# Kernel optimization log

Measured on AMD Instinct MI355X. Metric: run time of the kernel, lower is better.

The kernel has to match this reference:

```python
import jax, jax.numpy as jnp
import numpy as np

EPS = 1e-5
NPOINT, RADIUS, NSAMPLE, HEADS, DH = 512, 0.2, 64, 8, 64


def _ln(x, g, b):
    m = jnp.mean(x, -1, keepdims=True)
    v = jnp.var(x, -1, keepdims=True)
    return (x - m) * jax.lax.rsqrt(v + EPS) * g + b


def _gather(points, idx):
    # points [B,N,C], idx [B,...] -> [B,...,C]
    b = jnp.arange(points.shape[0]).reshape((-1,) + (1,) * (idx.ndim - 1))
    return points[b, idx]


def _fps(xyz, npoint):
    # farthest point sampling, deterministic start at index 0
    B, N, _ = xyz.shape

    def step(carry, _):
        dist, far = carry
        cen = jnp.take_along_axis(xyz, far[:, None, None], axis=1)  # [B,1,3]
        d = jnp.sum((xyz - cen) ** 2, -1)  # [B,N]
        dist = jnp.minimum(dist, d)
        nxt = jnp.argmax(dist, -1).astype(jnp.int32)
        return (dist, nxt), far

    init = (jnp.full((B, N), 1e10, xyz.dtype), jnp.zeros((B,), jnp.int32))
    _, idxs = jax.lax.scan(step, init, None, length=npoint)
    return idxs.T  # [B,npoint]


def _ball_query(xyz, new_xyz):
    # xyz [B,N,3], new_xyz [B,S,3] -> idx [B,S,NSAMPLE]
    N = xyz.shape[1]
    sq = (jnp.sum(new_xyz ** 2, -1)[:, :, None] + jnp.sum(xyz ** 2, -1)[:, None, :]
          - 2.0 * jnp.einsum('bsc,bnc->bsn', new_xyz, xyz))  # [B,S,N]
    gidx = jnp.broadcast_to(jnp.arange(N), sq.shape)
    gidx = jnp.where(sq > RADIUS ** 2, N, gidx)
    neg, _ = jax.lax.top_k(-gidx, NSAMPLE)  # smallest NSAMPLE valid indices
    idx = -neg
    return jnp.where(idx == N, idx[:, :, :1], idx)


def reference(features, sa_w0, sa_b0, sa_w1, sa_b1, sa_w2, sa_b2,
              bn_g0, bn_b0, bn_m0, bn_v0, bn_g1, bn_b1, bn_m1, bn_v1,
              bn_g2, bn_b2, bn_m2, bn_v2,
              lift_w, lift_b, lift_g, lift_beta, cls_token,
              qkv_w, out_w, out_b, ln1_g, ln1_b,
              pe_w1, pe_b1, pe_w2, pe_b2, ln2_g, ln2_b,
              ff_w1, ff_b1, ff_w2, ff_b2):
    B = features.shape[0]
    dim = cls_token.shape[0]
    xyz = jnp.transpose(features, (0, 2, 1))  # [B,N,3] (in_dim=3 so points==xyz)
    pts = xyz

    # ---- PointNet set abstraction ----
    fps_idx = _fps(xyz, NPOINT)
    new_xyz = _gather(xyz, fps_idx)  # [B,S,3]
    idx = _ball_query(xyz, new_xyz)  # [B,S,K]
    g_xyz = _gather(xyz, idx)  # [B,S,K,3]
    g_norm = g_xyz - new_xyz[:, :, None, :]
    g_pts = _gather(pts, idx)
    h = jnp.concatenate([g_norm, g_pts], -1)  # [B,S,K,6]
    h = jnp.transpose(h, (0, 3, 2, 1))  # [B,C,K,S]
    for (w, bb, g, be, m, v) in ((sa_w0, sa_b0, bn_g0, bn_b0, bn_m0, bn_v0),
                                 (sa_w1, sa_b1, bn_g1, bn_b1, bn_m1, bn_v1),
                                 (sa_w2, sa_b2, bn_g2, bn_b2, bn_m2, bn_v2)):
        h = jnp.einsum('bcks,oc->boks', h, w) + bb[None, :, None, None]
        h = (h - m[None, :, None, None]) * jax.lax.rsqrt(v[None, :, None, None] + EPS) \
            * g[None, :, None, None] + be[None, :, None, None]
        h = jax.nn.relu(h)
    feat = jnp.max(h, axis=2)  # [B,sa_dim,S]
    cent = jnp.transpose(new_xyz, (0, 2, 1))  # [B,3,S]

    # ---- lift ----
    x = jnp.einsum('bcs,oc->bos', jnp.concatenate([cent, feat], 1), lift_w) + lift_b[None, :, None]
    x = jnp.transpose(x, (0, 2, 1))  # [B,S,dim]
    x = _ln(x, lift_g, lift_beta)

    # ---- cls token + centroid deltas ----
    x = jnp.concatenate([jnp.broadcast_to(cls_token, (B, 1, dim)), x], 1)  # [B,n,dim]
    cent = jnp.concatenate([jnp.zeros((B, 3, 1), x.dtype), cent], -1)  # [B,3,n]
    delta = cent[:, :, :, None] - cent[:, :, None, :]  # [B,3,n,n]

    # ---- transformer ----
    scale = DH ** -0.5
    depth = qkv_w.shape[0]
    n = x.shape[1]
    for l in range(depth):
        h1 = _ln(x, ln1_g[l], ln1_b[l])
        qkv = h1 @ qkv_w[l]  # [B,n,3*inner]
        q, k, v = jnp.split(qkv, 3, -1)
        q = q.reshape(B, n, HEADS, DH).transpose(0, 2, 1, 3)
        k = k.reshape(B, n, HEADS, DH).transpose(0, 2, 1, 3)
        v = v.reshape(B, n, HEADS, DH).transpose(0, 2, 1, 3)
        pe = jax.nn.relu(jnp.einsum('bcij,oc->boij', delta, pe_w1[l]) + pe_b1[l][None, :, None, None])
        pe = jnp.einsum('bcij,oc->boij', pe, pe_w2[l]) + pe_b2[l][None, :, None, None]  # [B,1,n,n]
        dots = (jnp.einsum('bhid,bhjd->bhij', q, k) + pe) * scale
        attn = jax.nn.softmax(dots, -1)
        o = jnp.einsum('bhij,bhjd->bhid', attn, v).transpose(0, 2, 1, 3).reshape(B, n, HEADS * DH)
        x = x + (o @ out_w[l] + out_b[l])
        h2 = _ln(x, ln2_g[l], ln2_b[l])
        x = x + (jax.nn.gelu(h2 @ ff_w1[l] + ff_b1[l], approximate=False) @ ff_w2[l] + ff_b2[l])
    return x[:, 0]


def setup_inputs() -> dict:
    key = jax.random.key(0)
    ks = iter(jax.random.split(key, 64))

    def rnd(shape, s=0.02):
        return (jax.random.normal(next(ks), shape, jnp.float32) * s)

    D, dim, inner, mlp, sad = 6, 512, 512, 1024, 256
    inp = {}
    inp['features'] = jax.random.uniform(next(ks), (2, 3, 10000), jnp.float32, -1.0, 1.0)
    inp['sa_w0'] = rnd((64, 6), 0.2); inp['sa_b0'] = jnp.zeros((64,), jnp.float32)
    inp['sa_w1'] = rnd((64, 64), 0.1); inp['sa_b1'] = jnp.zeros((64,), jnp.float32)
    inp['sa_w2'] = rnd((sad, 64), 0.1); inp['sa_b2'] = jnp.zeros((sad,), jnp.float32)
    for i, c in ((0, 64), (1, 64), (2, sad)):
        inp[f'bn_g{i}'] = jnp.ones((c,), jnp.float32)
        inp[f'bn_b{i}'] = jnp.zeros((c,), jnp.float32)
        inp[f'bn_m{i}'] = jnp.zeros((c,), jnp.float32)
        inp[f'bn_v{i}'] = jnp.ones((c,), jnp.float32)
    inp['lift_w'] = rnd((dim, sad + 3), 0.05)
    inp['lift_b'] = jnp.zeros((dim,), jnp.float32)
    inp['lift_g'] = jnp.ones((dim,), jnp.float32)
    inp['lift_beta'] = jnp.zeros((dim,), jnp.float32)
    inp['cls_token'] = rnd((dim,), 1.0)
    inp['qkv_w'] = rnd((D, dim, 3 * inner))
    inp['out_w'] = rnd((D, inner, dim))
    inp['out_b'] = jnp.zeros((D, dim), jnp.float32)
    inp['ln1_g'] = jnp.ones((D, dim), jnp.float32)
    inp['ln1_b'] = jnp.zeros((D, dim), jnp.float32)
    inp['pe_w1'] = rnd((D, 64, 3), 0.1)
    inp['pe_b1'] = jnp.zeros((D, 64), jnp.float32)
    inp['pe_w2'] = rnd((D, 1, 64), 0.1)
    inp['pe_b2'] = jnp.zeros((D, 1), jnp.float32)
    inp['ln2_g'] = jnp.ones((D, dim), jnp.float32)
    inp['ln2_b'] = jnp.zeros((D, dim), jnp.float32)
    inp['ff_w1'] = rnd((D, dim, mlp))
    inp['ff_b1'] = jnp.zeros((D, mlp), jnp.float32)
    inp['ff_w2'] = rnd((D, mlp, dim))
    inp['ff_b2'] = jnp.zeros((D, dim), jnp.float32)
    return inp
```

## Files before the change

kernel.cpp:

```cpp
#include <hip/hip_runtime.h>
#include <math.h>

#define NPTS 10000
#define NP   512
#define NS   64
#define NTOK 513
#define DIM  512
#define NHEADS 8
#define DH   64
#define DEPTH 6
#define SAD  256
#define MLPD 1024
#define EPSV 1e-5f
#define PEB  2057

typedef float  f32x2  __attribute__((ext_vector_type(2)));
typedef float  f32x4  __attribute__((ext_vector_type(4)));
typedef __bf16 bf16x8 __attribute__((ext_vector_type(8)));
typedef unsigned short u16x4 __attribute__((ext_vector_type(4)));
typedef unsigned short u16x8 __attribute__((ext_vector_type(8)));

__device__ __forceinline__ unsigned short f2bf(float x) {
    unsigned u = __float_as_uint(x);
    unsigned r = u + 0x7fffu + ((u >> 16) & 1u);
    return (unsigned short)(r >> 16);
}
__device__ __forceinline__ bf16x8 bf8_from_f32(const float* p) {
    u16x8 h;
    #pragma unroll
    for (int e = 0; e < 8; e++) h[e] = f2bf(p[e]);
    return *(bf16x8*)&h;
}

__device__ __forceinline__ float blk_sum256(float v, float* red) {
    #pragma unroll
    for (int off = 32; off; off >>= 1) v += __shfl_down(v, off);
    __syncthreads();
    if ((threadIdx.x & 63) == 0) red[threadIdx.x >> 6] = v;
    __syncthreads();
    return red[0] + red[1] + red[2] + red[3];
}

__global__ __launch_bounds__(512, 1) void fps_wconv_kernel(
        const float* __restrict__ f, float* __restrict__ cent3,
        const float* __restrict__ qkv_w, unsigned short* __restrict__ qkvT,
        const float* __restrict__ out_w, unsigned short* __restrict__ outT,
        const float* __restrict__ ff_w1, unsigned short* __restrict__ ff1T,
        const float* __restrict__ ff_w2, unsigned short* __restrict__ ff2T) {
    #pragma clang fp contract(off)
    __shared__ union {
        struct {
            float pts[3 * 10240];
            unsigned long long spk[2][8];
        } fps;
        unsigned short tl[64][65];
    } sh;

    if (blockIdx.x >= 2) {
        int id = blockIdx.x - 2;
        const float* Ws; unsigned short* Wd; int K, N, tn, per;
        if (id < 1152)      { Ws = qkv_w; Wd = qkvT; K = 512;  N = 1536; tn = 24; per = 192; }
        else if (id < 1536) { id -= 1152; Ws = out_w; Wd = outT; K = 512; N = 512; tn = 8;  per = 64;  }
        else if (id < 2304) { id -= 1536; Ws = ff_w1; Wd = ff1T; K = 512; N = 1024; tn = 16; per = 128; }
        else                { id -= 2304; Ws = ff_w2; Wd = ff2T; K = 1024; N = 512; tn = 8;  per = 128; }
        const int l = id / per, rem = id % per;
        const int n0 = (rem % tn) * 64, k0 = (rem / tn) * 64;
        Ws += (size_t)l * K * N;
        Wd += (size_t)l * K * N;
        const int ty = threadIdx.x >> 4, c4 = (threadIdx.x & 15) * 4;
        #pragma unroll
        for (int i = 0; i < 2; i++) {
            int r = ty + 32 * i;
            f32x4 v = *(const f32x4*)(Ws + (size_t)(k0 + r) * N + n0 + c4);
            sh.tl[c4 + 0][r] = f2bf(v.x);
            sh.tl[c4 + 1][r] = f2bf(v.y);
            sh.tl[c4 + 2][r] = f2bf(v.z);
            sh.tl[c4 + 3][r] = f2bf(v.w);
        }
        __syncthreads();
        #pragma unroll
        for (int i = 0; i < 2; i++) {
            int r = ty + 32 * i;
            u16x4 hv = { sh.tl[r][c4], sh.tl[r][c4 + 1], sh.tl[r][c4 + 2], sh.tl[r][c4 + 3] };
            *(u16x4*)(Wd + (size_t)(n0 + r) * K + k0 + c4) = hv;
        }
        return;
    }

    const int b = blockIdx.x;
    const float* fx = f + (size_t)b * 3 * NPTS;
    const float* fy = fx + NPTS;
    const float* fz = fx + 2 * NPTS;
    const int t = threadIdx.x;
    const int wv = t >> 6, lane = t & 63;

    float* lx = sh.fps.pts;
    float* ly = sh.fps.pts + 10240;
    float* lz = sh.fps.pts + 20480;
    for (int p = t; p < NPTS; p += 512) {
        lx[p] = fx[p]; ly[p] = fy[p]; lz[p] = fz[p];
    }

    f32x2 px[10], py[10], pz[10], dist[10];
    #pragma unroll
    for (int q = 0; q < 10; q++) {
        #pragma unroll
        for (int e = 0; e < 2; e++) {
            int p = t + (2 * q + e) * 512;
            if (p < NPTS) { px[q][e] = fx[p]; py[q][e] = fy[p]; pz[q][e] = fz[p]; dist[q][e] = 1e10f; }
            else          { px[q][e] = 0.f;  py[q][e] = 0.f;  pz[q][e] = 0.f;  dist[q][e] = -1.0f; }
        }
    }
    if (t == 0) {
        float* c0 = cent3 + (size_t)b * NTOK * 3;
        c0[0] = 0.f; c0[1] = 0.f; c0[2] = 0.f;
    }
    float cx = fx[0], cy = fy[0], cz = fz[0];
    __syncthreads();

    for (int it = 0; it < NP; ++it) {
        if (t == 0) {
            float* c = cent3 + (size_t)(b * NTOK + 1 + it) * 3;
            c[0] = cx; c[1] = cy; c[2] = cz;
        }
        const f32x2 c2x = {cx, cx}, c2y = {cy, cy}, c2z = {cz, cz};
        float av[20]; unsigned ai[20];
        #pragma unroll
        for (int q = 0; q < 10; q++) {
            f32x2 dx = px[q] - c2x;
            f32x2 dy = py[q] - c2y;
            f32x2 dz = pz[q] - c2z;
            f32x2 s1 = dx * dx;
            f32x2 s2 = dy * dy;
            f32x2 s3 = dz * dz;
            f32x2 d  = (s1 + s2) + s3;
            f32x2 nd = __builtin_elementwise_min(dist[q], d);
            dist[q] = nd;
            av[2 * q]     = nd.x; ai[2 * q]     = (unsigned)(t + (2 * q) * 512);
            av[2 * q + 1] = nd.y; ai[2 * q + 1] = (unsigned)(t + (2 * q + 1) * 512);
        }
        #define CMB(a, bq) if (av[bq] > av[a]) { av[a] = av[bq]; ai[a] = ai[bq]; }
        #pragma unroll
        for (int i = 0; i < 10; i++) CMB(i, i + 10)
        #pragma unroll
        for (int i = 0; i < 5; i++) CMB(i, i + 5)
        CMB(0, 1) CMB(2, 3) CMB(0, 2) CMB(0, 4)
        #undef CMB
        float bv = av[0]; unsigned bi = ai[0];
        #define DSTEP(CTRL, RM) { \
            int _ov = __builtin_amdgcn_update_dpp(__float_as_int(bv), __float_as_int(bv), CTRL, RM, 0xF, false); \
            int _oi = __builtin_amdgcn_update_dpp((int)bi, (int)bi, CTRL, RM, 0xF, false); \
            float ov = __int_as_float(_ov); unsigned oi = (unsigned)_oi; \
            bool take = (ov > bv) || (ov == bv && oi < bi); \
            bv = take ? ov : bv; bi = take ? oi : bi; \
        }
        DSTEP(0x111, 0xF)
        DSTEP(0x112, 0xF)
        DSTEP(0x114, 0xF)
        DSTEP(0x118, 0xF)
        DSTEP(0x142, 0xA)
        DSTEP(0x143, 0xC)
        #undef DSTEP
        const int cur = it & 1;
        if (lane == 63) {
            sh.fps.spk[cur][wv] = ((unsigned long long)__float_as_uint(bv) << 32)
                                | (unsigned long long)(~bi);
        }
        __syncthreads();
        unsigned long long g = sh.fps.spk[cur][0];
        #pragma unroll
        for (int w = 1; w < 8; w++) {
            unsigned long long o = sh.fps.spk[cur][w];
            g = (o > g) ? o : g;
        }
        const unsigned widx = ~(unsigned)g;
        cx = lx[widx]; cy = ly[widx]; cz = lz[widx];
    }
}

__global__ __launch_bounds__(256) void ballmlp_pe_kernel(
        const float* __restrict__ f, const float* __restrict__ cent3,
        const float* __restrict__ w0, const float* __restrict__ b0,
        const float* __restrict__ g0, const float* __restrict__ be0,
        const float* __restrict__ m0, const float* __restrict__ v0,
        const float* __restrict__ w1, const float* __restrict__ b1,
        const float* __restrict__ g1, const float* __restrict__ be1,
        const float* __restrict__ m1, const float* __restrict__ v1,
        const float* __restrict__ w2, const float* __restrict__ b2,
        const float* __restrict__ g2, const float* __restrict__ be2,
        const float* __restrict__ m2, const float* __restrict__ v2,
        float* __restrict__ featb,
        const float* __restrict__ pw1_, const float* __restrict__ pb1_,
        const float* __restrict__ pw2_, const float* __restrict__ pb2_,
        float* __restrict__ pebuf) {
    if (blockIdx.x >= 2 * NP) {
        const int id = blockIdx.x - 2 * NP;
        const int l = id / PEB, rem = id % PEB;
        const float* pw1 = pw1_ + l * 192;
        const float* pb1 = pb1_ + l * 64;
        const float* pw2 = pw2_ + l * 64;
        const long total = 2L * NTOK * NTOK;
        long gid = (long)rem * 256 + threadIdx.x;
        if (gid >= total) return;
        int j = (int)(gid % NTOK);
        long r = gid / NTOK;
        int i = (int)(r % NTOK);
        int b = (int)(r / NTOK);
        const float* ci = cent3 + (size_t)(b * NTOK + i) * 3;
        const float* cj = cent3 + (size_t)(b * NTOK + j) * 3;
        float d0 = ci[0] - cj[0], d1 = ci[1] - cj[1], d2 = ci[2] - cj[2];
        float acc = pb2_[l];
        #pragma unroll 8
        for (int c = 0; c < 64; c++) {
            float tv = pw1[c * 3] * d0 + pw1[c * 3 + 1] * d1 + pw1[c * 3 + 2] * d2 + pb1[c];
            acc += pw2[c] * fmaxf(tv, 0.f);
        }
        pebuf[(size_t)l * total + gid] = acc;
        return;
    }

    const int bs = blockIdx.x;
    const int b = bs / NP, s = bs % NP;
    const int tid = threadIdx.x;
    const int wv = tid >> 6, lane = tid & 63;
    const int fr = lane & 15, fq = lane >> 4;

    __shared__ int sidx[NS];
    __shared__ alignas(16) unsigned short Xl[64][8];
    __shared__ alignas(16) unsigned short H1[64][72];
    __shared__ alignas(16) unsigned short H2[64][72];

    const float* fx = f + (size_t)b * 3 * NPTS;
    const float* fy = fx + NPTS;
    const float* fz = fx + 2 * NPTS;
    const float* c  = cent3 + (size_t)(b * NTOK + 1 + s) * 3;
    const float nx = c[0], ny = c[1], nz = c[2];

    const int c1 = 16 * wv + fr;
    const float sc0 = g0[c1] / sqrtf(v0[c1] + EPSV);
    const float off0 = (b0[c1] - m0[c1]) * sc0 + be0[c1];
    const float sc1 = g1[c1] / sqrtf(v1[c1] + EPSV);
    const float off1 = (b1[c1] - m1[c1]) * sc1 + be1[c1];

    u16x8 b0h = {0,0,0,0,0,0,0,0};
    if (fq == 0) {
        const float* wr = w0 + c1 * 6;
        #pragma unroll
        for (int e = 0; e < 6; e++) b0h[e] = f2bf(wr[e]);
    }
    bf16x8 bf0 = *(bf16x8*)&b0h;
    bf16x8 bf1[2];
    #pragma unroll
    for (int ks = 0; ks < 2; ks++)
        bf1[ks] = bf8_from_f32(w1 + (size_t)c1 * 64 + ks * 32 + fq * 8);

    if (wv == 0) {
        const float nn = __fadd_rn(__fadd_rn(__fmul_rn(nx, nx), __fmul_rn(ny, ny)), __fmul_rn(nz, nz));
        int cnt = 0, first = -1;
        for (int base = 0; base < NPTS; base += 64) {
            const int p = base + lane;
            bool valid = false;
            if (p < NPTS) {
                float x = fx[p], y = fy[p], z = fz[p];
                float pp = __fadd_rn(__fadd_rn(__fmul_rn(x, x), __fmul_rn(y, y)), __fmul_rn(z, z));
                float dt = __fadd_rn(__fadd_rn(__fmul_rn(nx, x), __fmul_rn(ny, y)), __fmul_rn(nz, z));
                float sq = __fsub_rn(__fadd_rn(nn, pp), __fmul_rn(2.0f, dt));
                valid = !(sq > 0.04f);
            }
            unsigned long long m = __ballot(valid);
            if (first < 0 && m) first = base + __builtin_ctzll(m);
            int pos = cnt + __popcll(m & ((1ull << lane) - 1ull));
            if (valid && pos < NS) sidx[pos] = p;
            cnt += __popcll(m);
            if (cnt >= NS) break;
        }
        for (int pos = cnt + lane; pos < NS; pos += 64) sidx[pos] = first;
    }
    __syncthreads();

    if (tid < 64) {
        const int p = sidx[tid];
        float i3 = fx[p], i4 = fy[p], i5 = fz[p];
        u16x8 xv;
        xv[0] = f2bf(i3 - nx); xv[1] = f2bf(i4 - ny); xv[2] = f2bf(i5 - nz);
        xv[3] = f2bf(i3); xv[4] = f2bf(i4); xv[5] = f2bf(i5);
        xv[6] = 0; xv[7] = 0;
        *(u16x8*)(&Xl[tid][0]) = xv;
    }
    __syncthreads();

    const u16x8 z8 = {0,0,0,0,0,0,0,0};
    const bf16x8 zf = *(const bf16x8*)&z8;

    #pragma unroll
    for (int m = 0; m < 4; m++) {
        bf16x8 af = (fq == 0) ? *(const bf16x8*)(&Xl[m * 16 + fr][0]) : zf;
        f32x4 d = (f32x4){0.f, 0.f, 0.f, 0.f};
        d = __builtin_amdgcn_mfma_f32_16x16x32_bf16(af, bf0, d, 0, 0, 0);
        #pragma unroll
        for (int j = 0; j < 4; j++) {
            float v = fmaxf(d[j] * sc0 + off0, 0.f);
            H1[m * 16 + fq * 4 + j][16 * wv + fr] = f2bf(v);
        }
    }
    __syncthreads();

    #pragma unroll
    for (int m = 0; m < 4; m++) {
        f32x4 d = (f32x4){0.f, 0.f, 0.f, 0.f};
        #pragma unroll
        for (int ks = 0; ks < 2; ks++) {
            bf16x8 af = *(const bf16x8*)(&H1[m * 16 + fr][ks * 32 + fq * 8]);
            d = __builtin_amdgcn_mfma_f32_16x16x32_bf16(af, bf1[ks], d, 0, 0, 0);
        }
        #pragma unroll
        for (int j = 0; j < 4; j++) {
            float v = fmaxf(d[j] * sc1 + off1, 0.f);
            H2[m * 16 + fq * 4 + j][16 * wv + fr] = f2bf(v);
        }
    }
    __syncthreads();

    bf16x8 af2[4][2];
    #pragma unroll
    for (int m = 0; m < 4; m++)
        #pragma unroll
        for (int ks = 0; ks < 2; ks++)
            af2[m][ks] = *(const bf16x8*)(&H2[m * 16 + fr][ks * 32 + fq * 8]);

    float* outp = featb + (size_t)bs * SAD;
    #pragma unroll
    for (int t = 0; t < 4; t++) {
        const int c2 = 64 * wv + 16 * t + fr;
        const float sc2 = g2[c2] / sqrtf(v2[c2] + EPSV);
        const float off2 = (b2[c2] - m2[c2]) * sc2 + be2[c2];
        bf16x8 bf2[2];
        #pragma unroll
        for (int ks = 0; ks < 2; ks++)
            bf2[ks] = bf8_from_f32(w2 + (size_t)c2 * 64 + ks * 32 + fq * 8);
        float mx = -INFINITY;
        #pragma unroll
        for (int m = 0; m < 4; m++) {
            f32x4 d = (f32x4){0.f, 0.f, 0.f, 0.f};
            d = __builtin_amdgcn_mfma_f32_16x16x32_bf16(af2[m][0], bf2[0], d, 0, 0, 0);
            d = __builtin_amdgcn_mfma_f32_16x16x32_bf16(af2[m][1], bf2[1], d, 0, 0, 0);
            #pragma unroll
            for (int j = 0; j < 4; j++)
                mx = fmaxf(mx, fmaxf(d[j] * sc2 + off2, 0.f));
        }
        mx = fmaxf(mx, __shfl_xor(mx, 16));
        mx = fmaxf(mx, __shfl_xor(mx, 32));
        if (fq == 0) outp[c2] = mx;
    }
}

__global__ __launch_bounds__(256) void lift_ln_kernel(const float* __restrict__ cent3,
                                                      const float* __restrict__ featb,
                                                      const float* __restrict__ lw,
                                                      const float* __restrict__ lb,
                                                      const float* __restrict__ lg,
                                                      const float* __restrict__ lbeta,
                                                      const float* __restrict__ cls,
                                                      float* __restrict__ x) {
    const int t = threadIdx.x;
    if (blockIdx.x < 2) {
        int b = blockIdx.x;
        x[(size_t)(b * NTOK) * DIM + t]       = cls[t];
        x[(size_t)(b * NTOK) * DIM + t + 256] = cls[t + 256];
        return;
    }
    const int bs = blockIdx.x - 2;
    const int b = bs / NP, s = bs % NP;
    __shared__ float si[259];
    __shared__ float sy[512];
    __shared__ float red[4];
    if (t < 3) si[t] = cent3[(size_t)(b * NTOK + 1 + s) * 3 + t];
    si[3 + t] = featb[(size_t)bs * SAD + t];
    __syncthreads();
    for (int o = t; o < DIM; o += 256) {
        const float* wr = lw + (size_t)o * 259;
        float acc = lb[o];
        for (int ci = 0; ci < 259; ci++) acc += wr[ci] * si[ci];
        sy[o] = acc;
    }
    __syncthreads();
    float tot  = blk_sum256(sy[t] + sy[t + 256], red);
    float mean = tot * (1.0f / 512.0f);
    float d0 = sy[t] - mean, d1 = sy[t + 256] - mean;
    float var = blk_sum256(d0 * d0 + d1 * d1, red) * (1.0f / 512.0f);
    float inv = 1.0f / sqrtf(var + EPSV);
    float* xr = x + (size_t)(b * NTOK + 1 + s) * DIM;
    xr[t]       = d0 * inv * lg[t]       + lbeta[t];
    xr[t + 256] = d1 * inv * lg[t + 256] + lbeta[t + 256];
}

__global__ __launch_bounds__(256) void ln_kernel(const float* __restrict__ xin,
                                                 const float* __restrict__ g,
                                                 const float* __restrict__ beta,
                                                 unsigned short* __restrict__ y) {
    const int r = blockIdx.x;
    const float* xr = xin + (size_t)r * DIM;
    const int t = threadIdx.x;
    float a0 = xr[t], a1 = xr[t + 256];
    __shared__ float red[4];
    float mean = blk_sum256(a0 + a1, red) * (1.0f / 512.0f);
    float d0 = a0 - mean, d1 = a1 - mean;
    float var = blk_sum256(d0 * d0 + d1 * d1, red) * (1.0f / 512.0f);
    float inv = 1.0f / sqrtf(var + EPSV);
    unsigned short* yr = y + (size_t)r * DIM;
    yr[t]       = f2bf(d0 * inv * g[t]       + beta[t]);
    yr[t + 256] = f2bf(d1 * inv * g[t + 256] + beta[t + 256]);
}

__global__ __launch_bounds__(256) void attn_mfma_kernel(const unsigned short* __restrict__ qkv,
                                                        const float* __restrict__ pebuf,
                                                        unsigned short* __restrict__ obuf) {
    __shared__ alignas(16) unsigned short Qs[64][72];
    __shared__ alignas(16) unsigned short Ks[64][72];
    __shared__ alignas(16) unsigned short Vt[64][72];
    __shared__ alignas(16) unsigned short Ps[64][72];

    const int ti = blockIdx.x;
    const int bh = blockIdx.y;
    const int b = bh >> 3, h = bh & 7;
    const int i0 = ti * 64;
    const int tid = threadIdx.x;
    const int w = tid >> 6, lane = tid & 63;
    const int fr = lane & 15, fq = lane >> 4;
    const int fko = fq * 8;

    const unsigned short* qbase = qkv + (size_t)b * NTOK * (3 * DIM) + h * DH;
    const int sr = tid >> 2, sc = (tid & 3) * 16;

    {
        int i = i0 + sr;
        u16x8 v0 = {0,0,0,0,0,0,0,0}, v1 = {0,0,0,0,0,0,0,0};
        if (i < NTOK) {
            v0 = *(const u16x8*)(qbase + (size_t)i * (3 * DIM) + sc);
            v1 = *(const u16x8*)(qbase + (size_t)i * (3 * DIM) + sc + 8);
        }
        *(u16x8*)(&Qs[sr][sc]) = v0;
        *(u16x8*)(&Qs[sr][sc + 8]) = v1;
    }

    float mrow[4], lrow[4];
    f32x4 od[4];
    #pragma unroll
    for (int r = 0; r < 4; r++) { mrow[r] = -INFINITY; lrow[r] = 0.f; }
    #pragma unroll
    for (int dt = 0; dt < 4; dt++) od[dt] = (f32x4){0.f, 0.f, 0.f, 0.f};

    const unsigned short* kbase = qkv + (size_t)b * NTOK * (3 * DIM) + DIM + h * DH;
    const unsigned short* vbase = qkv + (size_t)b * NTOK * (3 * DIM) + 2 * DIM + h * DH;

    for (int jc = 0; jc < 9; jc++) {
        const int j0 = jc * 64;
        const int wj = (NTOK - j0) < 64 ? (NTOK - j0) : 64;
        __syncthreads();
        if (sr < wj) {
            const unsigned short* kp = kbase + (size_t)(j0 + sr) * (3 * DIM) + sc;
            const unsigned short* vp = vbase + (size_t)(j0 + sr) * (3 * DIM) + sc;
            u16x8 k0 = *(const u16x8*)(kp);
            u16x8 k1 = *(const u16x8*)(kp + 8);
            *(u16x8*)(&Ks[sr][sc]) = k0;
            *(u16x8*)(&Ks[sr][sc + 8]) = k1;
            u16x8 q0 = *(const u16x8*)(vp);
            u16x8 q1 = *(const u16x8*)(vp + 8);
            #pragma unroll
            for (int e = 0; e < 8; e++) {
                Vt[sc + e][sr] = q0[e];
                Vt[sc + 8 + e][sr] = q1[e];
            }
        } else {
            u16x8 z = {0,0,0,0,0,0,0,0};
            *(u16x8*)(&Ks[sr][sc]) = z;
            *(u16x8*)(&Ks[sr][sc + 8]) = z;
            #pragma unroll
            for (int e = 0; e < 16; e++) Vt[sc + e][sr] = 0;
        }
        __syncthreads();

        bf16x8 qf0 = *(const bf16x8*)(&Qs[16 * w + fr][fko]);
        bf16x8 qf1 = *(const bf16x8*)(&Qs[16 * w + fr][fko + 32]);
        f32x4 sa[4];
        #pragma unroll
        for (int jt = 0; jt < 4; jt++) {
            f32x4 acc = (f32x4){0.f, 0.f, 0.f, 0.f};
            bf16x8 kf0 = *(const bf16x8*)(&Ks[jt * 16 + fr][fko]);
            bf16x8 kf1 = *(const bf16x8*)(&Ks[jt * 16 + fr][fko + 32]);
            acc = __builtin_amdgcn_mfma_f32_16x16x32_bf16(qf0, kf0, acc, 0, 0, 0);
            acc = __builtin_amdgcn_mfma_f32_16x16x32_bf16(qf1, kf1, acc, 0, 0, 0);
            sa[jt] = acc;
        }

        float sv[4][4];
        float cm[4] = {-INFINITY, -INFINITY, -INFINITY, -INFINITY};
        #pragma unroll
        for (int jt = 0; jt < 4; jt++) {
            int jl = jt * 16 + fr;
            int jg = j0 + jl; if (jg > NTOK - 1) jg = NTOK - 1;
            #pragma unroll
            for (int r = 0; r < 4; r++) {
                int i = i0 + 16 * w + fq * 4 + r; if (i > NTOK - 1) i = NTOK - 1;
                float pe = pebuf[((size_t)b * NTOK + i) * NTOK + jg];
                float s = (sa[jt][r] + pe) * 0.125f;
                s = (jl < wj) ? s : -INFINITY;
                sv[jt][r] = s;
                cm[r] = fmaxf(cm[r], s);
            }
        }
        #pragma unroll
        for (int off = 1; off < 16; off <<= 1) {
            #pragma unroll
            for (int r = 0; r < 4; r++) cm[r] = fmaxf(cm[r], __shfl_xor(cm[r], off));
        }
        float fac[4], rs[4];
        #pragma unroll
        for (int r = 0; r < 4; r++) {
            float mn = fmaxf(mrow[r], cm[r]);
            fac[r] = __expf(mrow[r] - mn);
            mrow[r] = mn;
            rs[r] = 0.f;
        }
        #pragma unroll
        for (int jt = 0; jt < 4; jt++) {
            #pragma unroll
            for (int r = 0; r < 4; r++) {
                float p = __expf(sv[jt][r] - mrow[r]);
                rs[r] += p;
                Ps[16 * w + fq * 4 + r][jt * 16 + fr] = f2bf(p);
            }
        }
        #pragma unroll
        for (int off = 1; off < 16; off <<= 1) {
            #pragma unroll
            for (int r = 0; r < 4; r++) rs[r] += __shfl_xor(rs[r], off);
        }
        #pragma unroll
        for (int r = 0; r < 4; r++) lrow[r] = lrow[r] * fac[r] + rs[r];
        #pragma unroll
        for (int dt = 0; dt < 4; dt++) {
            #pragma unroll
            for (int r = 0; r < 4; r++) od[dt][r] *= fac[r];
        }

        bf16x8 pf0 = *(const bf16x8*)(&Ps[16 * w + fr][fko]);
        bf16x8 pf1 = *(const bf16x8*)(&Ps[16 * w + fr][fko + 32]);
        #pragma unroll
        for (int dt = 0; dt < 4; dt++) {
            bf16x8 vf0 = *(const bf16x8*)(&Vt[dt * 16 + fr][fko]);
            bf16x8 vf1 = *(const bf16x8*)(&Vt[dt * 16 + fr][fko + 32]);
            od[dt] = __builtin_amdgcn_mfma_f32_16x16x32_bf16(pf0, vf0, od[dt], 0, 0, 0);
            od[dt] = __builtin_amdgcn_mfma_f32_16x16x32_bf16(pf1, vf1, od[dt], 0, 0, 0);
        }
    }

    #pragma unroll
    for (int r = 0; r < 4; r++) {
        int i = i0 + 16 * w + fq * 4 + r;
        if (i >= NTOK) continue;
        float inv = 1.0f / lrow[r];
        #pragma unroll
        for (int dt = 0; dt < 4; dt++) {
            obuf[((size_t)b * NTOK + i) * DIM + h * DH + dt * 16 + fr] = f2bf(od[dt][r] * inv);
        }
    }
}

template <int BM, int BN, int ACT, int OBF>
__global__ __launch_bounds__(256) void gemm_bt_kernel(const unsigned short* __restrict__ A,
                                                      const unsigned short* __restrict__ Bt,
                                                      const float* __restrict__ bias,
                                                      const float* __restrict__ resid,
                                                      void* __restrict__ Cv,
                                                      int M, int N, int K) {
    constexpr int FM = BM / 32, FN = BN / 32;
    __shared__ unsigned short Al[BM][72];
    __shared__ unsigned short Bl[BN][72];
    const int tid = threadIdx.x;
    const int bm = blockIdx.y * BM, bn = blockIdx.x * BN;
    const int wid = tid >> 6, lane = tid & 63;
    const int wr = (wid >> 1) * (BM / 2), wc = (wid & 1) * (BN / 2);
    const int fr = lane & 15, fko = (lane >> 4) * 8;
    const int srow = tid >> 3, sc8 = (tid & 7) * 8;

    f32x4 acc[FM][FN];
    #pragma unroll
    for (int m = 0; m < FM; m++)
        #pragma unroll
        for (int n = 0; n < FN; n++) acc[m][n] = (f32x4){0.f, 0.f, 0.f, 0.f};

    for (int kt = 0; kt < K; kt += 64) {
        #pragma unroll
        for (int q = 0; q < BM / 32; q++) {
            int r = srow + q * 32;
            int row = bm + r;
            u16x8 va = {0,0,0,0,0,0,0,0};
            if (row < M) va = *(const u16x8*)(A + (size_t)row * K + kt + sc8);
            *(u16x8*)(&Al[r][sc8]) = va;
        }
        #pragma unroll
        for (int q = 0; q < BN / 32; q++) {
            int r = srow + q * 32;
            u16x8 vb = *(const u16x8*)(Bt + (size_t)(bn + r) * K + kt + sc8);
            *(u16x8*)(&Bl[r][sc8]) = vb;
        }
        __syncthreads();
        #pragma unroll
        for (int ks = 0; ks < 2; ks++) {
            bf16x8 af[FM], bfr[FN];
            #pragma unroll
            for (int m = 0; m < FM; m++) af[m]  = *(const bf16x8*)(&Al[wr + m * 16 + fr][ks * 32 + fko]);
            #pragma unroll
            for (int n = 0; n < FN; n++) bfr[n] = *(const bf16x8*)(&Bl[wc + n * 16 + fr][ks * 32 + fko]);
            #pragma unroll
            for (int m = 0; m < FM; m++)
                #pragma unroll
                for (int n = 0; n < FN; n++)
                    acc[m][n] = __builtin_amdgcn_mfma_f32_16x16x32_bf16(af[m], bfr[n], acc[m][n], 0, 0, 0);
        }
        __syncthreads();
    }

    float* Cf = (float*)Cv;
    unsigned short* Cb = (unsigned short*)Cv;
    const int rg = (lane >> 4) * 4;
    #pragma unroll
    for (int m = 0; m < FM; m++) {
        #pragma unroll
        for (int n = 0; n < FN; n++) {
            int col = bn + wc + n * 16 + fr;
            float bv = bias ? bias[col] : 0.f;
            #pragma unroll
            for (int j = 0; j < 4; j++) {
                int row = bm + wr + m * 16 + rg + j;
                if (row >= M) continue;
                float v = acc[m][n][j] + bv;
                if (ACT == 1) v = 0.5f * v * (1.0f + erff(v * 0.70710678118654752f));
                if (resid) v += resid[(size_t)row * N + col];
                if (OBF) Cb[(size_t)row * N + col] = f2bf(v);
                else     Cf[(size_t)row * N + col] = v;
            }
        }
    }
}

__global__ void copyout_kernel(const float* __restrict__ x, float* __restrict__ out) {
    int t = blockIdx.x * 256 + threadIdx.x;
    if (t < 2 * DIM) {
        int b = t >> 9, d = t & 511;
        out[t] = x[(size_t)(b * NTOK) * DIM + d];
    }
}

extern "C" void kernel_launch(void* const* d_in, const int* in_sizes, int n_in,
                              void* d_out, int out_size, void* d_ws, size_t ws_size,
                              hipStream_t stream) {
    const float* f      = (const float*)d_in[0];
    const float* sa_w0  = (const float*)d_in[1];
    const float* sa_b0  = (const float*)d_in[2];
    const float* sa_w1  = (const float*)d_in[3];
    const float* sa_b1  = (const float*)d_in[4];
    const float* sa_w2  = (const float*)d_in[5];
    const float* sa_b2  = (const float*)d_in[6];
    const float* bn_g0  = (const float*)d_in[7];
    const float* bn_b0  = (const float*)d_in[8];
    const float* bn_m0  = (const float*)d_in[9];
    const float* bn_v0  = (const float*)d_in[10];
    const float* bn_g1  = (const float*)d_in[11];
    const float* bn_b1  = (const float*)d_in[12];
    const float* bn_m1  = (const float*)d_in[13];
    const float* bn_v1  = (const float*)d_in[14];
    const float* bn_g2  = (const float*)d_in[15];
    const float* bn_b2  = (const float*)d_in[16];
    const float* bn_m2  = (const float*)d_in[17];
    const float* bn_v2  = (const float*)d_in[18];
    const float* lift_w = (const float*)d_in[19];
    const float* lift_b = (const float*)d_in[20];
    const float* lift_g = (const float*)d_in[21];
    const float* lift_be= (const float*)d_in[22];
    const float* cls    = (const float*)d_in[23];
    const float* qkv_w  = (const float*)d_in[24];
    const float* out_w  = (const float*)d_in[25];
    const float* out_b  = (const float*)d_in[26];
    const float* ln1_g  = (const float*)d_in[27];
    const float* ln1_b  = (const float*)d_in[28];
    const float* pe_w1  = (const float*)d_in[29];
    const float* pe_b1  = (const float*)d_in[30];
    const float* pe_w2  = (const float*)d_in[31];
    const float* pe_b2  = (const float*)d_in[32];
    const float* ln2_g  = (const float*)d_in[33];
    const float* ln2_b  = (const float*)d_in[34];
    const float* ff_w1  = (const float*)d_in[35];
    const float* ff_b1  = (const float*)d_in[36];
    const float* ff_w2  = (const float*)d_in[37];
    const float* ff_b2  = (const float*)d_in[38];

    char* ws = (char*)d_ws;
    size_t off = 0;
    auto alloc = [&](size_t bytes) -> char* {
        char* p = ws + off;
        off = (off + bytes + 255) & ~(size_t)255;
        return p;
    };
    float* cent3 = (float*)alloc((size_t)2 * NTOK * 3 * 4);
    float* featb = (float*)alloc((size_t)2 * NP * SAD * 4);
    float* xbuf  = (float*)alloc((size_t)2 * NTOK * DIM * 4);
    unsigned short* h1buf = (unsigned short*)alloc((size_t)2 * NTOK * DIM * 2);
    unsigned short* qkvb  = (unsigned short*)alloc((size_t)2 * NTOK * 3 * DIM * 2);
    unsigned short* obuf  = (unsigned short*)alloc((size_t)2 * NTOK * DIM * 2);
    unsigned short* hff   = (unsigned short*)alloc((size_t)2 * NTOK * MLPD * 2);
    float* pebuf = (float*)alloc((size_t)DEPTH * 2 * NTOK * NTOK * 4);
    unsigned short* qkvT = (unsigned short*)alloc((size_t)DEPTH * 3 * DIM * DIM * 2);
    unsigned short* outT = (unsigned short*)alloc((size_t)DEPTH * DIM * DIM * 2);
    unsigned short* ff1T = (unsigned short*)alloc((size_t)DEPTH * DIM * MLPD * 2);
    unsigned short* ff2T = (unsigned short*)alloc((size_t)DEPTH * MLPD * DIM * 2);

    fps_wconv_kernel<<<3074, 512, 0, stream>>>(f, cent3,
        qkv_w, qkvT, out_w, outT, ff_w1, ff1T, ff_w2, ff2T);
    ballmlp_pe_kernel<<<2 * NP + DEPTH * PEB, 256, 0, stream>>>(f, cent3,
        sa_w0, sa_b0, bn_g0, bn_b0, bn_m0, bn_v0,
        sa_w1, sa_b1, bn_g1, bn_b1, bn_m1, bn_v1,
        sa_w2, sa_b2, bn_g2, bn_b2, bn_m2, bn_v2, featb,
        pe_w1, pe_b1, pe_w2, pe_b2, pebuf);
    lift_ln_kernel<<<2 * NP + 2, 256, 0, stream>>>(cent3, featb, lift_w, lift_b, lift_g, lift_be, cls, xbuf);

    const int M = 2 * NTOK;
    const int GY = (M + 63) / 64;
    const size_t peL = 2L * NTOK * NTOK;
    for (int l = 0; l < DEPTH; l++) {
        ln_kernel<<<M, 256, 0, stream>>>(xbuf, ln1_g + l * DIM, ln1_b + l * DIM, h1buf);
        gemm_bt_kernel<64, 64, 0, 1><<<dim3(24, GY), 256, 0, stream>>>(
            h1buf, qkvT + (size_t)l * 3 * DIM * DIM, nullptr, nullptr, qkvb, M, 3 * DIM, DIM);
        attn_mfma_kernel<<<dim3(9, 16), 256, 0, stream>>>(qkvb, pebuf + (size_t)l * peL, obuf);
        gemm_bt_kernel<64, 32, 0, 0><<<dim3(16, GY), 256, 0, stream>>>(
            obuf, outT + (size_t)l * DIM * DIM, out_b + l * DIM, xbuf, xbuf, M, DIM, DIM);
        ln_kernel<<<M, 256, 0, stream>>>(xbuf, ln2_g + l * DIM, ln2_b + l * DIM, h1buf);
        gemm_bt_kernel<64, 64, 1, 1><<<dim3(16, GY), 256, 0, stream>>>(
            h1buf, ff1T + (size_t)l * DIM * MLPD, ff_b1 + l * MLPD, nullptr, hff, M, MLPD, DIM);
        gemm_bt_kernel<64, 32, 0, 0><<<dim3(16, GY), 256, 0, stream>>>(
            hff, ff2T + (size_t)l * MLPD * DIM, ff_b2 + l * DIM, xbuf, xbuf, M, DIM, MLPD);
    }
    copyout_kernel<<<4, 256, 0, stream>>>(xbuf, (float*)d_out);
}
```

Baseline: 1.333 ms.

## Fuse LayerNorm into the QKV and FF1 GEMMs; buffer FPS centroids in LDS

Removes the standalone LayerNorm kernels. Each GEMM block now computes per-row mean and variance over its 64 rows, then normalises and converts the fp32 activations to bf16 while loading its A tile. This saves 12 launches and the round trip through the bf16 intermediate buffer, but every column block recomputes the row statistics and reads fp32 activations instead of bf16. It also uses a one-pass variance, which is less numerically robust. In the FPS loop, centroids are kept in shared memory and written to global memory once at the end, instead of a global store per iteration.

Result: slower. 1.422 ms (+6.7%).

```diff
diff --git a/kernel.cpp b/kernel.cpp
--- a/kernel.cpp
+++ b/kernel.cpp
@@ -51,6 +51,7 @@
     __shared__ union {
         struct {
             float pts[3 * 10240];
+            float centb[NP * 3];
             unsigned long long spk[2][8];
         } fps;
         unsigned short tl[64][65];
@@ -111,17 +112,14 @@
             else          { px[q][e] = 0.f;  py[q][e] = 0.f;  pz[q][e] = 0.f;  dist[q][e] = -1.0f; }
         }
     }
-    if (t == 0) {
-        float* c0 = cent3 + (size_t)b * NTOK * 3;
-        c0[0] = 0.f; c0[1] = 0.f; c0[2] = 0.f;
-    }
     float cx = fx[0], cy = fy[0], cz = fz[0];
     __syncthreads();
 
     for (int it = 0; it < NP; ++it) {
         if (t == 0) {
-            float* c = cent3 + (size_t)(b * NTOK + 1 + it) * 3;
-            c[0] = cx; c[1] = cy; c[2] = cz;
+            sh.fps.centb[it * 3 + 0] = cx;
+            sh.fps.centb[it * 3 + 1] = cy;
+            sh.fps.centb[it * 3 + 2] = cz;
         }
         const f32x2 c2x = {cx, cx}, c2y = {cy, cy}, c2z = {cz, cz};
         float av[20]; unsigned ai[20];
@@ -176,6 +174,10 @@
         const unsigned widx = ~(unsigned)g;
         cx = lx[widx]; cy = ly[widx]; cz = lz[widx];
     }
+
+    float* cb = cent3 + (size_t)b * NTOK * 3;
+    if (t < 3) cb[t] = 0.f;
+    for (int i = t; i < NP * 3; i += 512) cb[3 + i] = sh.fps.centb[i];
 }
 
 __global__ __launch_bounds__(256) void ballmlp_pe_kernel(
@@ -394,24 +396,6 @@
     xr[t + 256] = d1 * inv * lg[t + 256] + lbeta[t + 256];
 }
 
-__global__ __launch_bounds__(256) void ln_kernel(const float* __restrict__ xin,
-                                                 const float* __restrict__ g,
-                                                 const float* __restrict__ beta,
-                                                 unsigned short* __restrict__ y) {
-    const int r = blockIdx.x;
-    const float* xr = xin + (size_t)r * DIM;
-    const int t = threadIdx.x;
-    float a0 = xr[t], a1 = xr[t + 256];
-    __shared__ float red[4];
-    float mean = blk_sum256(a0 + a1, red) * (1.0f / 512.0f);
-    float d0 = a0 - mean, d1 = a1 - mean;
-    float var = blk_sum256(d0 * d0 + d1 * d1, red) * (1.0f / 512.0f);
-    float inv = 1.0f / sqrtf(var + EPSV);
-    unsigned short* yr = y + (size_t)r * DIM;
-    yr[t]       = f2bf(d0 * inv * g[t]       + beta[t]);
-    yr[t + 256] = f2bf(d1 * inv * g[t + 256] + beta[t + 256]);
-}
-
 __global__ __launch_bounds__(256) void attn_mfma_kernel(const unsigned short* __restrict__ qkv,
                                                         const float* __restrict__ pebuf,
                                                         unsigned short* __restrict__ obuf) {
@@ -640,6 +624,121 @@
                 if (resid) v += resid[(size_t)row * N + col];
                 if (OBF) Cb[(size_t)row * N + col] = f2bf(v);
                 else     Cf[(size_t)row * N + col] = v;
+            }
+        }
+    }
+}
+
+template <int BN, int ACT>
+__global__ __launch_bounds__(256) void gemm_ln_bt_kernel(
+        const float* __restrict__ X,
+        const float* __restrict__ lg, const float* __restrict__ lbe,
+        const unsigned short* __restrict__ Bt,
+        const float* __restrict__ bias,
+        unsigned short* __restrict__ C,
+        int M, int N, int K) {
+    constexpr int FM = 2, FN = BN / 32;
+    __shared__ unsigned short Al[64][72];
+    __shared__ unsigned short Bl[BN][72];
+    __shared__ float ps[64][4], pq[64][4];
+    __shared__ float smean[64], sinv[64];
+    const int tid = threadIdx.x;
+    const int bm = blockIdx.y * 64, bn = blockIdx.x * BN;
+    const int wid = tid >> 6, lane = tid & 63;
+    const int wr = (wid >> 1) * 32, wc = (wid & 1) * (BN / 2);
+    const int fr = lane & 15, fko = (lane >> 4) * 8;
+    const int srow = tid >> 3, sc8 = (tid & 7) * 8;
+
+    {
+        const int r = tid & 63, part = tid >> 6;
+        const int row = bm + r;
+        float s = 0.f, sq = 0.f;
+        if (row < M) {
+            const float* xr = X + (size_t)row * K + part * (K / 4);
+            for (int c = 0; c < K / 4; c += 4) {
+                f32x4 v = *(const f32x4*)(xr + c);
+                s  += (v.x + v.y) + (v.z + v.w);
+                sq += (v.x * v.x + v.y * v.y) + (v.z * v.z + v.w * v.w);
+            }
+        }
+        ps[r][part] = s; pq[r][part] = sq;
+    }
+    __syncthreads();
+    if (tid < 64) {
+        float s  = (ps[tid][0] + ps[tid][1]) + (ps[tid][2] + ps[tid][3]);
+        float sq = (pq[tid][0] + pq[tid][1]) + (pq[tid][2] + pq[tid][3]);
+        float mean = s / (float)K;
+        float var = fmaxf(sq / (float)K - mean * mean, 0.f);
+        smean[tid] = mean;
+        sinv[tid] = 1.0f / sqrtf(var + EPSV);
+    }
+    __syncthreads();
+
+    f32x4 acc[FM][FN];
+    #pragma unroll
+    for (int m = 0; m < FM; m++)
+        #pragma unroll
+        for (int n = 0; n < FN; n++) acc[m][n] = (f32x4){0.f, 0.f, 0.f, 0.f};
+
+    for (int kt = 0; kt < K; kt += 64) {
+        float gv[8], bev[8];
+        *(f32x4*)(gv)      = *(const f32x4*)(lg  + kt + sc8);
+        *(f32x4*)(gv + 4)  = *(const f32x4*)(lg  + kt + sc8 + 4);
+        *(f32x4*)(bev)     = *(const f32x4*)(lbe + kt + sc8);
+        *(f32x4*)(bev + 4) = *(const f32x4*)(lbe + kt + sc8 + 4);
+        #pragma unroll
+        for (int q = 0; q < 2; q++) {
+            int r = srow + q * 32;
+            int row = bm + r;
+            float xe[8] = {0,0,0,0,0,0,0,0};
+            if (row < M) {
+                *(f32x4*)(xe)     = *(const f32x4*)(X + (size_t)row * K + kt + sc8);
+                *(f32x4*)(xe + 4) = *(const f32x4*)(X + (size_t)row * K + kt + sc8 + 4);
+            }
+            const float mean = smean[r], inv = sinv[r];
+            u16x8 hv;
+            #pragma unroll
+            for (int e = 0; e < 8; e++)
+                hv[e] = f2bf((xe[e] - mean) * inv * gv[e] + bev[e]);
+            *(u16x8*)(&Al[r][sc8]) = hv;
+        }
+        #pragma unroll
+        for (int q = 0; q < BN / 32; q++) {
+            int r = srow + q * 32;
+            u16x8 vb = *(const u16x8*)(Bt + (size_t)(bn + r) * K + kt + sc8);
+            *(u16x8*)(&Bl[r][sc8]) = vb;
+        }
+        __syncthreads();
+        #pragma unroll
+        for (int ks = 0; ks < 2; ks++) {
+            bf16x8 af[FM], bfr[FN];
+            #pragma unroll
+            for (int m = 0; m < FM; m++) af[m]  = *(const bf16x8*)(&Al[wr + m * 16 + fr][ks * 32 + fko]);
+            #pragma unroll
+            for (int n = 0; n < FN; n++) bfr[n] = *(const bf16x8*)(&Bl[wc + n * 16 + fr][ks * 32 + fko]);
+            #pragma unroll
+            for (int m = 0; m < FM; m++)
+                #pragma unroll
+                for (int n = 0; n < FN; n++)
+                    acc[m][n] = __builtin_amdgcn_mfma_f32_16x16x32_bf16(af[m], bfr[n], acc[m][n], 0, 0, 0);
+        }
+        __syncthreads();
+    }
+
+    const int rg = (lane >> 4) * 4;
+    #pragma unroll
+    for (int m = 0; m < FM; m++) {
+        #pragma unroll
+        for (int n = 0; n < FN; n++) {
+            int col = bn + wc + n * 16 + fr;
+            float bv = bias ? bias[col] : 0.f;
+            #pragma unroll
+            for (int j = 0; j < 4; j++) {
+                int row = bm + wr + m * 16 + rg + j;
+                if (row >= M) continue;
+                float v = acc[m][n][j] + bv;
+                if (ACT == 1) v = 0.5f * v * (1.0f + erff(v * 0.70710678118654752f));
+                C[(size_t)row * N + col] = f2bf(v);
             }
         }
     }
@@ -706,7 +805,6 @@
     float* cent3 = (float*)alloc((size_t)2 * NTOK * 3 * 4);
     float* featb = (float*)alloc((size_t)2 * NP * SAD * 4);
     float* xbuf  = (float*)alloc((size_t)2 * NTOK * DIM * 4);
-    unsigned short* h1buf = (unsigned short*)alloc((size_t)2 * NTOK * DIM * 2);
     unsigned short* qkvb  = (unsigned short*)alloc((size_t)2 * NTOK * 3 * DIM * 2);
     unsigned short* obuf  = (unsigned short*)alloc((size_t)2 * NTOK * DIM * 2);
     unsigned short* hff   = (unsigned short*)alloc((size_t)2 * NTOK * MLPD * 2);
@@ -729,15 +827,15 @@
     const int GY = (M + 63) / 64;
     const size_t peL = 2L * NTOK * NTOK;
     for (int l = 0; l < DEPTH; l++) {
-        ln_kernel<<<M, 256, 0, stream>>>(xbuf, ln1_g + l * DIM, ln1_b + l * DIM, h1buf);
-        gemm_bt_kernel<64, 64, 0, 1><<<dim3(24, GY), 256, 0, stream>>>(
-            h1buf, qkvT + (size_t)l * 3 * DIM * DIM, nullptr, nullptr, qkvb, M, 3 * DIM, DIM);
+        gemm_ln_bt_kernel<64, 0><<<dim3(24, GY), 256, 0, stream>>>(
+            xbuf, ln1_g + l * DIM, ln1_b + l * DIM,
+            qkvT + (size_t)l * 3 * DIM * DIM, nullptr, qkvb, M, 3 * DIM, DIM);
         attn_mfma_kernel<<<dim3(9, 16), 256, 0, stream>>>(qkvb, pebuf + (size_t)l * peL, obuf);
         gemm_bt_kernel<64, 32, 0, 0><<<dim3(16, GY), 256, 0, stream>>>(
             obuf, outT + (size_t)l * DIM * DIM, out_b + l * DIM, xbuf, xbuf, M, DIM, DIM);
-        ln_kernel<<<M, 256, 0, stream>>>(xbuf, ln2_g + l * DIM, ln2_b + l * DIM, h1buf);
-        gemm_bt_kernel<64, 64, 1, 1><<<dim3(16, GY), 256, 0, stream>>>(
-            h1buf, ff1T + (size_t)l * DIM * MLPD, ff_b1 + l * MLPD, nullptr, hff, M, MLPD, DIM);
+        gemm_ln_bt_kernel<64, 1><<<dim3(16, GY), 256, 0, stream>>>(
+            xbuf, ln2_g + l * DIM, ln2_b + l * DIM,
+            ff1T + (size_t)l * DIM * MLPD, ff_b1 + l * MLPD, hff, M, MLPD, DIM);
         gemm_bt_kernel<64, 32, 0, 0><<<dim3(16, GY), 256, 0, stream>>>(
             hff, ff2T + (size_t)l * MLPD * DIM, ff_b2 + l * DIM, xbuf, xbuf, M, DIM, MLPD);
     }
```
